# Optimization experiments

Hardware: AMD Instinct MI355X
Metric: run time of the kernel (lower is better)

## Reference

```python
import jax, jax.numpy as jnp
import numpy as np

D = 512          # latent_dim
H = 8            # num_heads
NLAYERS = 8
DFF = 8          # fast_transformers d_ff slot receives num_heads in the repo (kept faithful)
NC = 10          # NUM_CLUSTERS
KMEANS_ITERS = 10
NJ, NF, T, BS = 25, 6, 1024, 16
NCLS, MAXA = 12, 6


def _pe(S, d):
    pos = jnp.arange(S, dtype=jnp.float32)[:, None]
    div = jnp.exp(jnp.arange(0, d, 2, dtype=jnp.float32) * (-np.log(10000.0) / d))
    pe = jnp.zeros((S, d), jnp.float32)
    pe = pe.at[:, 0::2].set(jnp.sin(pos * div))
    pe = pe.at[:, 1::2].set(jnp.cos(pos * div))
    return pe


def _ln(x, g, b, eps=1e-5):
    m = jnp.mean(x, -1, keepdims=True)
    v = jnp.var(x, -1, keepdims=True)
    return (x - m) * jax.lax.rsqrt(v + eps) * g + b


def _clustered_attn_one(q, k, v):
    # q, k, v: (L, Dh). Cluster queries (Lloyd k-means, deterministic init from
    # first NC queries), attend with centroids, broadcast back to queries.
    cent = q[:NC]
    for _ in range(KMEANS_ITERS):
        d = jnp.sum(cent * cent, -1)[None, :] - 2.0 * (q @ cent.T)  # (L, C)
        a = jnp.argmin(d, -1)
        oh = jax.nn.one_hot(a, NC, dtype=q.dtype)                   # (L, C)
        cent = (oh.T @ q) / jnp.maximum(oh.sum(0), 1.0)[:, None]
    d = jnp.sum(cent * cent, -1)[None, :] - 2.0 * (q @ cent.T)
    a = jnp.argmin(d, -1)                                           # (L,)
    temp = 1.0 / np.sqrt(q.shape[-1])
    A = jax.nn.softmax((cent @ k.T) * temp, -1)                     # (C, L)
    return (A @ v)[a]                                               # (L, Dh)


def _layer(z, Wq, bq, Wk, bk, Wv, bv, Wo, bo, g1, c1, g2, c2, W1, b1, W2, b2):
    B, S, d = z.shape
    Dh = d // H
    q = (z @ Wq + bq).reshape(B, S, H, Dh).transpose(0, 2, 1, 3).reshape(B * H, S, Dh)
    k = (z @ Wk + bk).reshape(B, S, H, Dh).transpose(0, 2, 1, 3).reshape(B * H, S, Dh)
    v = (z @ Wv + bv).reshape(B, S, H, Dh).transpose(0, 2, 1, 3).reshape(B * H, S, Dh)
    o = jax.vmap(_clustered_attn_one)(q, k, v)
    o = o.reshape(B, H, S, Dh).transpose(0, 2, 1, 3).reshape(B, S, d)
    z = z + (o @ Wo + bo)                     # post-norm TransformerEncoderLayer
    z = _ln(z, g1, c1)
    y = jax.nn.relu(z @ W1 + b1) @ W2 + b2    # d_ff == num_heads (repo bug, kept)
    return _ln(z + y, g2, c2)


def _forward(x, muQuery, sigmaQuery, mu_w, mu_b, sig_w, sig_b, skel_w, skel_b,
             Wq, bq, Wk, bk, Wv, bv, Wo, bo, g1, c1, g2, c2, W1, b1, W2, b2, y):
    bs, nj, nf, nframes = x.shape
    h = x.transpose(3, 0, 1, 2).reshape(nframes, bs, nj * nf) @ skel_w + skel_b  # (T,B,D)
    mu_enc = muQuery[y].reshape(bs, -1) @ mu_w + mu_b          # (B, D)
    sig_enc = sigmaQuery[y].reshape(bs, -1) @ sig_w + sig_b    # (B, D)
    xseq = jnp.concatenate([mu_enc[None], sig_enc[None], h], 0)  # (S, B, D)
    S = xseq.shape[0]
    xseq = xseq + _pe(S, xseq.shape[-1])[:, None, :]
    z = xseq.transpose(1, 0, 2)  # (B, S, D): attend over the sequence axis
    for i in range(NLAYERS):
        z = _layer(z, Wq[i], bq[i], Wk[i], bk[i], Wv[i], bv[i], Wo[i], bo[i],
                   g1[i], c1[i], g2[i], c2[i], W1[i], b1[i], W2[i], b2[i])
    out = z.transpose(1, 0, 2)  # (S, B, D)
    return out[0], out[1]       # mu, logvar: (B, D) each


def setup_inputs() -> dict:
    key = jax.random.key(0)
    ks = jax.random.split(key, 20)
    s = 0.02
    return {
        "x": jax.random.normal(ks[0], (BS, NJ, NF, T), jnp.float32),
        "y": jax.random.randint(ks[1], (BS, MAXA), 0, NCLS),
        "mask": jnp.ones((BS, T), bool),
        "muQuery": jax.random.normal(ks[2], (NCLS, D), jnp.float32),
        "sigmaQuery": jax.random.normal(ks[3], (NCLS + 1, D), jnp.float32),
        "mu_w": jax.random.normal(ks[4], (D * MAXA, D), jnp.float32) * s,
        "mu_b": jnp.zeros((D,), jnp.float32),
        "sig_w": jax.random.normal(ks[5], (D * MAXA, D), jnp.float32) * s,
        "sig_b": jnp.zeros((D,), jnp.float32),
        "skel_w": jax.random.normal(ks[6], (NJ * NF, D), jnp.float32) * s,
        "skel_b": jnp.zeros((D,), jnp.float32),
        "Wq": jax.random.normal(ks[7], (NLAYERS, D, D), jnp.float32) * s,
        "bq": jnp.zeros((NLAYERS, D), jnp.float32),
        "Wk": jax.random.normal(ks[8], (NLAYERS, D, D), jnp.float32) * s,
        "bk": jnp.zeros((NLAYERS, D), jnp.float32),
        "Wv": jax.random.normal(ks[9], (NLAYERS, D, D), jnp.float32) * s,
        "bv": jnp.zeros((NLAYERS, D), jnp.float32),
        "Wo": jax.random.normal(ks[10], (NLAYERS, D, D), jnp.float32) * s,
        "bo": jnp.zeros((NLAYERS, D), jnp.float32),
        "g1": jnp.ones((NLAYERS, D), jnp.float32),
        "c1": jnp.zeros((NLAYERS, D), jnp.float32),
        "g2": jnp.ones((NLAYERS, D), jnp.float32),
        "c2": jnp.zeros((NLAYERS, D), jnp.float32),
        "W1": jax.random.normal(ks[11], (NLAYERS, D, DFF), jnp.float32) * s,
        "b1": jnp.zeros((NLAYERS, DFF), jnp.float32),
        "W2": jax.random.normal(ks[12], (NLAYERS, DFF, D), jnp.float32) * s,
        "b2": jnp.zeros((NLAYERS, D), jnp.float32),
    }


def reference(x, y, mask, muQuery, sigmaQuery, mu_w, mu_b, sig_w, sig_b,
              skel_w, skel_b, Wq, bq, Wk, bk, Wv, bv, Wo, bo,
              g1, c1, g2, c2, W1, b1, W2, b2):
    del mask  # computed but never passed to the encoder in the original code
    mu, logvar = _forward(x, muQuery, sigmaQuery, mu_w, mu_b, sig_w, sig_b,
                          skel_w, skel_b, Wq, bq, Wk, bk, Wv, bv, Wo, bo,
                          g1, c1, g2, c2, W1, b1, W2, b2, y)
    return mu, logvar
```

## Files before the change

### kernel.cpp

```cpp
#include <hip/hip_runtime.h>
#include <hip/hip_fp16.h>
#include <math.h>

#define D 512
#define H 8
#define DH 64
#define NLAYERS 8
#define DFF 8
#define NC 10
#define KITERS 10
#define SEQ 1026
#define SEQP 1032
#define BATCH 16
#define MR (BATCH*SEQ)
#define NBUF ((size_t)MR * D)
#define DD ((size_t)D * D)
#define NBH (BATCH*H)
#define KSPLIT 64
#define KCH 48

typedef _Float16 f16;
typedef f16 f16x8 __attribute__((ext_vector_type(8)));
typedef float f32x4 __attribute__((ext_vector_type(4)));

__device__ __forceinline__ void split2(float x, float y, unsigned& uh, unsigned& ul) {
    __half hx = __float2half_rn(x), hy = __float2half_rn(y);
    __half lx = __float2half_rn(x - __half2float(hx));
    __half ly = __float2half_rn(y - __half2float(hy));
    uh = (unsigned)__half_as_ushort(hx) | ((unsigned)__half_as_ushort(hy) << 16);
    ul = (unsigned)__half_as_ushort(lx) | ((unsigned)__half_as_ushort(ly) << 16);
}

__device__ __forceinline__ float pe_val(int s, int d) {
    float e = (float)(d & ~1);
    float dv = expf(e * (-9.210340371976184f / 512.0f));
    float ph = (float)s * dv;
    return (d & 1) ? cosf(ph) : sinf(ph);
}

__launch_bounds__(256)
__global__ void convert_w(const float* __restrict__ Wq, const float* __restrict__ Wk,
                          const float* __restrict__ Wv,
                          ushort* __restrict__ whiT, ushort* __restrict__ wloT)
{
    __shared__ float tile[64][65];
    const int tid = threadIdx.x;
    const int k0 = blockIdx.x * 64, n0 = blockIdx.y * 64, m = blockIdx.z;
    const int which = m % 3, lyr = m / 3;
    const float* base;
    switch (which) { case 0: base = Wq; break; case 1: base = Wk; break;
                     default: base = Wv; }
    const float* W = base + (size_t)lyr * DD;
    {
        int r = tid >> 4, c = (tid & 15) * 4;
        #pragma unroll
        for (int p = 0; p < 4; ++p) {
            float4 v = *(const float4*)&W[(size_t)(k0 + r + p*16)*D + n0 + c];
            tile[r + p*16][c]   = v.x; tile[r + p*16][c+1] = v.y;
            tile[r + p*16][c+2] = v.z; tile[r + p*16][c+3] = v.w;
        }
    }
    __syncthreads();
    ushort* ohp = whiT + (size_t)m * DD;
    ushort* olp = wloT + (size_t)m * DD;
    {
        int nl = tid >> 3, kc = (tid & 7) * 8;
        #pragma unroll
        for (int p = 0; p < 2; ++p) {
            int n = nl + p*32;
            uint4 UH, UL;
            split2(tile[kc+0][n], tile[kc+1][n], UH.x, UL.x);
            split2(tile[kc+2][n], tile[kc+3][n], UH.y, UL.y);
            split2(tile[kc+4][n], tile[kc+5][n], UH.z, UL.z);
            split2(tile[kc+6][n], tile[kc+7][n], UH.w, UL.w);
            size_t off = (size_t)(n0 + n)*D + k0 + kc;
            *(uint4*)&ohp[off] = UH;
            *(uint4*)&olp[off] = UL;
        }
    }
}

__launch_bounds__(256)
__global__ void embed_ms_part(const int* __restrict__ y,
    const float* __restrict__ muQ, const float* __restrict__ sigQ,
    const float* __restrict__ mu_w, const float* __restrict__ sig_w,
    float* __restrict__ pbuf)
{
    __shared__ float xs[BATCH][KCH];
    const int tid = threadIdx.x;
    const int kc = blockIdx.x, p = blockIdx.y;
    const float* Q = p ? sigQ : muQ;
    const float* W = p ? sig_w : mu_w;
    for (int i = tid; i < BATCH*KCH; i += 256) {
        int b = i / KCH, k = i - b*KCH;
        int gk = kc*KCH + k;
        int a = y[b*6 + (gk >> 9)];
        xs[b][k] = Q[a*D + (gk & 511)];
    }
    __syncthreads();
    const int n0 = tid*2;
    float a0[BATCH], a1[BATCH];
    #pragma unroll
    for (int b = 0; b < BATCH; ++b) { a0[b] = 0.f; a1[b] = 0.f; }
    #pragma unroll 4
    for (int k = 0; k < KCH; ++k) {
        const float2 wv = *(const float2*)&W[(size_t)(kc*KCH + k)*D + n0];
        #pragma unroll
        for (int b = 0; b < BATCH; ++b) {
            float xv = xs[b][k];
            a0[b] += xv * wv.x;
            a1[b] += xv * wv.y;
        }
    }
    float* pp = pbuf + ((size_t)(p*KSPLIT + kc)*BATCH)*D;
    #pragma unroll
    for (int b = 0; b < BATCH; ++b)
        *(float2*)&pp[(size_t)b*D + n0] = make_float2(a0[b], a1[b]);
}

__launch_bounds__(256)
__global__ void embed_ms_reduce(const float* __restrict__ pbuf,
    const float* __restrict__ mu_b, const float* __restrict__ sig_b,
    float* __restrict__ z)
{
    const int tid = threadIdx.x;
    const int p = blockIdx.x, b = blockIdx.y;
    const float* bb = p ? sig_b : mu_b;
    #pragma unroll
    for (int half = 0; half < 2; ++half) {
        const int d = tid + half*256;
        float s = bb[d];
        const float* pp = pbuf + ((size_t)(p*KSPLIT)*BATCH + b)*D + d;
        #pragma unroll 8
        for (int kc = 0; kc < KSPLIT; ++kc)
            s += pp[(size_t)kc*BATCH*D];
        z[((size_t)b*SEQ + p)*D + d] = s + pe_val(p, d);
    }
}

__launch_bounds__(256)
__global__ void embed_kernel(const float* __restrict__ x,
    const float* __restrict__ skel_w, const float* __restrict__ skel_b,
    float* __restrict__ z)
{
    __shared__ float xin[600];
    const int bx = blockIdx.x, b = blockIdx.y, tid = threadIdx.x;
    const int f0 = bx * 4;
    for (int idx = tid; idx < 600; idx += 256) {
        int i = idx >> 2, ff = idx & 3;
        xin[idx] = x[((size_t)(b*150 + i))*1024 + f0 + ff];
    }
    __syncthreads();
    const float4* x4 = (const float4*)xin;
    for (int dd = 0; dd < 2; ++dd) {
        const int d = tid + dd*256;
        float a0, a1, a2, a3;
        a0 = a1 = a2 = a3 = skel_b[d];
        for (int i = 0; i < 150; ++i) {
            float4 xv = x4[i];
            float w = skel_w[(size_t)i*D + d];
            a0 += xv.x*w; a1 += xv.y*w; a2 += xv.z*w; a3 += xv.w*w;
        }
        float a[4] = {a0, a1, a2, a3};
        #pragma unroll
        for (int ff = 0; ff < 4; ++ff) {
            int s = f0 + ff + 2;
            z[((size_t)b*SEQ + s)*D + d] = a[ff] + pe_val(s, d);
        }
    }
}

__launch_bounds__(256)
__global__ void gemm_qkv(const float* __restrict__ A,
                         const ushort* __restrict__ Bhi_b, const ushort* __restrict__ Blo_b,
                         const float* __restrict__ bq, const float* __restrict__ bk,
                         const float* __restrict__ bv,
                         float* __restrict__ outbase, int M)
{
    __shared__ ushort Ah[128*40], Al[128*40], Bh[128*40], Bl[128*40];
    const int tid = threadIdx.x;
    const int m0 = blockIdx.y * 128, n0 = blockIdx.x * 128;
    const int zz = blockIdx.z;
    const ushort* Bhi = Bhi_b + (size_t)zz * DD;
    const ushort* Blo = Blo_b + (size_t)zz * DD;
    const float* bias = (zz == 0) ? bq : (zz == 1) ? bk : bv;
    float* out = outbase + (size_t)zz * NBUF;
    const int l = tid & 63, wv = tid >> 6;
    const int wr = wv >> 1, wc = wv & 1;

    f32x4 acc[4][4];
    #pragma unroll
    for (int mi = 0; mi < 4; ++mi)
        #pragma unroll
        for (int ni = 0; ni < 4; ++ni) acc[mi][ni] = (f32x4){0.f, 0.f, 0.f, 0.f};

    const int ar_s = tid >> 1, ac_s = (tid & 1) * 16;
    const bool va = (m0 + ar_s) < M;
    const int r0 = (tid*2) >> 2,   kc0 = ((tid*2) & 3) * 8;
    const int r1 = (tid*2+1) >> 2, kc1 = ((tid*2+1) & 3) * 8;
    const float4 fz = make_float4(0.f, 0.f, 0.f, 0.f);

    for (int kt = 0; kt < 16; ++kt) {
        const int kb = kt * 32;
        float4 a0 = fz, a1 = fz, a2 = fz, a3 = fz;
        if (va) {
            const float4* ap = (const float4*)&A[(size_t)(m0 + ar_s)*D + kb + ac_s];
            a0 = ap[0]; a1 = ap[1]; a2 = ap[2]; a3 = ap[3];
        }
        uint4 bh0 = *(const uint4*)&Bhi[(size_t)(n0+r0)*D + kb + kc0];
        uint4 bh1 = *(const uint4*)&Bhi[(size_t)(n0+r1)*D + kb + kc1];
        uint4 bl0 = *(const uint4*)&Blo[(size_t)(n0+r0)*D + kb + kc0];
        uint4 bl1 = *(const uint4*)&Blo[(size_t)(n0+r1)*D + kb + kc1];

        uint4 AH0, AL0, AH1, AL1;
        split2(a0.x, a0.y, AH0.x, AL0.x); split2(a0.z, a0.w, AH0.y, AL0.y);
        split2(a1.x, a1.y, AH0.z, AL0.z); split2(a1.z, a1.w, AH0.w, AL0.w);
        split2(a2.x, a2.y, AH1.x, AL1.x); split2(a2.z, a2.w, AH1.y, AL1.y);
        split2(a3.x, a3.y, AH1.z, AL1.z); split2(a3.z, a3.w, AH1.w, AL1.w);

        if (kt) __syncthreads();
        *(uint4*)&Ah[ar_s*40 + ac_s]     = AH0;
        *(uint4*)&Ah[ar_s*40 + ac_s + 8] = AH1;
        *(uint4*)&Al[ar_s*40 + ac_s]     = AL0;
        *(uint4*)&Al[ar_s*40 + ac_s + 8] = AL1;
        *(uint4*)&Bh[r0*40 + kc0] = bh0;  *(uint4*)&Bh[r1*40 + kc1] = bh1;
        *(uint4*)&Bl[r0*40 + kc0] = bl0;  *(uint4*)&Bl[r1*40 + kc1] = bl1;
        __syncthreads();

        const int ko = (l >> 4) * 8;
        f16x8 bhf[4], blf[4];
        #pragma unroll
        for (int ni = 0; ni < 4; ++ni) {
            int br = wc*64 + ni*16 + (l & 15);
            bhf[ni] = *(const f16x8*)&Bh[br*40 + ko];
            blf[ni] = *(const f16x8*)&Bl[br*40 + ko];
        }
        #pragma unroll
        for (int mi = 0; mi < 4; ++mi) {
            int ar = wr*64 + mi*16 + (l & 15);
            f16x8 ahf = *(const f16x8*)&Ah[ar*40 + ko];
            f16x8 alf = *(const f16x8*)&Al[ar*40 + ko];
            #pragma unroll
            for (int ni = 0; ni < 4; ++ni) {
                acc[mi][ni] = __builtin_amdgcn_mfma_f32_16x16x32_f16(ahf, bhf[ni], acc[mi][ni], 0, 0, 0);
                acc[mi][ni] = __builtin_amdgcn_mfma_f32_16x16x32_f16(ahf, blf[ni], acc[mi][ni], 0, 0, 0);
                acc[mi][ni] = __builtin_amdgcn_mfma_f32_16x16x32_f16(alf, bhf[ni], acc[mi][ni], 0, 0, 0);
            }
        }
    }

    const int col_base = n0 + wc*64 + (l & 15);
    const int row_base = m0 + wr*64 + ((l >> 4) << 2);
    #pragma unroll
    for (int ni = 0; ni < 4; ++ni) {
        const int col = col_base + ni*16;
        const float bv2 = bias[col];
        #pragma unroll
        for (int mi = 0; mi < 4; ++mi) {
            #pragma unroll
            for (int e = 0; e < 4; ++e) {
                const int row = row_base + mi*16 + e;
                if (row >= M) continue;
                float val = acc[mi][ni][e] + bv2;
                int bb = row / SEQ;
                int ss = row - bb*SEQ;
                int hh = col >> 6, dh = col & 63;
                out[((size_t)(bb*H + hh)*SEQ + ss)*DH + dh] = val;
            }
        }
    }
}

__launch_bounds__(1024, 4)
__global__ void attn_kernel(const float* __restrict__ q, const float* __restrict__ kk,
                            const float* __restrict__ v,
                            float* __restrict__ centout, unsigned char* __restrict__ assignout)
{
    __shared__ float At[NC][SEQP];
    __shared__ float cent[NC][DH];
    __shared__ float tailrow[2][DH];
    __shared__ float cnorm[NC];
    __shared__ int   cnt[NC];
    __shared__ int   chg;
    __shared__ unsigned char assign[1028];
    __shared__ float redA[16][NC];
    __shared__ float redB[16][NC];
    __shared__ float Mc[NC];
    __shared__ float Sinv[NC];

    const int tid = threadIdx.x;
    const int wv = tid >> 6, lane = tid & 63;
    const int bh = blockIdx.x;
    const float* qh = q  + (size_t)bh * SEQ * DH;
    const float* kh = kk + (size_t)bh * SEQ * DH;
    const float* vh = v  + (size_t)bh * SEQ * DH;
    float* part = &At[0][0];

    if (tid < NC*DH) ((float*)cent)[tid] = qh[tid];
    if (tid >= NC*DH && tid < NC*DH + 2*DH) ((float*)tailrow)[tid - NC*DH] = qh[1024*DH + (tid - NC*DH)];
    __syncthreads();

    const float4* qrow4 = (const float4*)(qh + (size_t)tid * DH);
    int prev_a = -1, prev_t = -1;

    for (int iter = 0; iter <= KITERS; ++iter) {
        if (tid < NC) {
            float sn = 0.f;
            #pragma unroll
            for (int i = 0; i < 16; ++i) {
                float4 cv = *(const float4*)&cent[tid][i*4];
                sn += cv.x*cv.x + cv.y*cv.y + cv.z*cv.z + cv.w*cv.w;
            }
            cnorm[tid] = sn;
            cnt[tid] = 0;
        }
        if (tid == 0) chg = 0;
        __syncthreads();

        int a_reg;
        {
            float acc[NC];
            #pragma unroll
            for (int c = 0; c < NC; ++c) acc[c] = 0.f;
            #pragma unroll 8
            for (int kq = 0; kq < 16; ++kq) {
                float4 qv = qrow4[kq];
                #pragma unroll
                for (int c = 0; c < NC; ++c) {
                    float4 cv = *(const float4*)&cent[c][kq*4];
                    acc[c] += qv.x*cv.x + qv.y*cv.y + qv.z*cv.z + qv.w*cv.w;
                }
            }
            int best = 0; float bd = 1e30f;
            #pragma unroll
            for (int c = 0; c < NC; ++c) {
                float dd = cnorm[c] - 2.f*acc[c];
                if (dd < bd) { bd = dd; best = c; }
            }
            a_reg = best;
            assign[tid] = (unsigned char)best;
        }
        {
            unsigned long long mm = __ballot(a_reg != prev_a);
            if (lane == 0 && mm) atomicAdd(&chg, 1);
            prev_a = a_reg;
        }
        if (iter < KITERS) {
            #pragma unroll
            for (int c = 0; c < NC; ++c) {
                unsigned long long m = __ballot(a_reg == c);
                if (lane == 0 && m) atomicAdd(&cnt[c], __popcll(m));
            }
        }
        if (tid < 2) {
            int best = 0; float bd = 1e30f;
            #pragma unroll
            for (int c = 0; c < NC; ++c) {
                float acc = 0.f;
                #pragma unroll
                for (int i = 0; i < 64; ++i) acc += tailrow[tid][i]*cent[c][i];
                float dd = cnorm[c] - 2.f*acc;
                if (dd < bd) { bd = dd; best = c; }
            }
            assign[1024 + tid] = (unsigned char)best;
            if (best != prev_t) atomicAdd(&chg, 1);
            prev_t = best;
            if (iter < KITERS) atomicAdd(&cnt[best], 1);
        }
        __syncthreads();
        if (iter == KITERS) break;
        if (chg == 0) break;

        {
            float accq[NC];
            #pragma unroll
            for (int c = 0; c < NC; ++c) accq[c] = 0.f;
            const int s0 = wv * 64;
            #pragma unroll 8
            for (int i = 0; i < 64; ++i) {
                int s = s0 + i;
                float qv = qh[(size_t)s*DH + lane];
                int c = assign[s];
                #pragma unroll
                for (int cc = 0; cc < NC; ++cc) accq[cc] += (cc == c) ? qv : 0.f;
            }
            if (wv < 2) {
                int c = assign[1024 + wv];
                float qv = tailrow[wv][lane];
                #pragma unroll
                for (int cc = 0; cc < NC; ++cc) accq[cc] += (cc == c) ? qv : 0.f;
            }
            #pragma unroll
            for (int c = 0; c < NC; ++c) part[(wv*NC + c)*DH + lane] = accq[c];
        }
        __syncthreads();
        if (tid < NC*DH) {
            int c = tid >> 6;
            float s = 0.f;
            #pragma unroll
            for (int w = 0; w < 16; ++w) s += part[w*(NC*DH) + tid];
            ((float*)cent)[tid] = s / fmaxf((float)cnt[c], 1.f);
        }
        __syncthreads();
    }

    if (tid < 2*DH) ((float*)tailrow)[tid] = kh[1024*DH + tid];
    __syncthreads();

    float lg[NC], lgt[NC];
    {
        const float4* krow4 = (const float4*)(kh + (size_t)tid * DH);
        #pragma unroll
        for (int c = 0; c < NC; ++c) lg[c] = 0.f;
        #pragma unroll 8
        for (int kq = 0; kq < 16; ++kq) {
            float4 kv = krow4[kq];
            #pragma unroll
            for (int c = 0; c < NC; ++c) {
                float4 cv = *(const float4*)&cent[c][kq*4];
                lg[c] += kv.x*cv.x + kv.y*cv.y + kv.z*cv.z + kv.w*cv.w;
            }
        }
        #pragma unroll
        for (int c = 0; c < NC; ++c) lg[c] *= 0.125f;
    }
    if (tid < 2) {
        #pragma unroll
        for (int c = 0; c < NC; ++c) {
            float acc = 0.f;
            #pragma unroll
            for (int i = 0; i < 64; ++i) acc += tailrow[tid][i]*cent[c][i];
            lgt[c] = 0.125f * acc;
        }
    }

    #pragma unroll
    for (int c = 0; c < NC; ++c) {
        float m = lg[c];
        if (tid < 2) m = fmaxf(m, lgt[c]);
        #pragma unroll
        for (int off = 32; off; off >>= 1) m = fmaxf(m, __shfl_xor(m, off, 64));
        if (lane == 0) redA[wv][c] = m;
    }
    __syncthreads();
    if (tid < NC) {
        float m = redA[0][tid];
        #pragma unroll
        for (int w = 1; w < 16; ++w) m = fmaxf(m, redA[w][tid]);
        Mc[tid] = m;
    }
    __syncthreads();
    #pragma unroll
    for (int c = 0; c < NC; ++c) lg[c] = expf(lg[c] - Mc[c]);
    if (tid < 2) {
        #pragma unroll
        for (int c = 0; c < NC; ++c) lgt[c] = expf(lgt[c] - Mc[c]);
    }
    #pragma unroll
    for (int c = 0; c < NC; ++c) {
        float s = lg[c] + ((tid < 2) ? lgt[c] : 0.f);
        #pragma unroll
        for (int off = 32; off; off >>= 1) s += __shfl_xor(s, off, 64);
        if (lane == 0) redB[wv][c] = s;
    }
    __syncthreads();
    if (tid < NC) {
        float s = 0.f;
        #pragma unroll
        for (int w = 0; w < 16; ++w) s += redB[w][tid];
        Sinv[tid] = 1.f / s;
    }
    __syncthreads();
    #pragma unroll
    for (int c = 0; c < NC; ++c) At[c][tid] = lg[c] * Sinv[c];
    if (tid < 2) {
        #pragma unroll
        for (int c = 0; c < NC; ++c) At[c][1024 + tid] = lgt[c] * Sinv[c];
    }
    __syncthreads();

    {
        float accv[NC];
        #pragma unroll
        for (int c = 0; c < NC; ++c) accv[c] = 0.f;
        const int s0 = wv * 64;
        for (int i = 0; i < 64; i += 4) {
            float vv0 = vh[(size_t)(s0+i  )*DH + lane];
            float vv1 = vh[(size_t)(s0+i+1)*DH + lane];
            float vv2 = vh[(size_t)(s0+i+2)*DH + lane];
            float vv3 = vh[(size_t)(s0+i+3)*DH + lane];
            #pragma unroll
            for (int c = 0; c < NC; ++c) {
                float4 av = *(const float4*)&At[c][s0+i];
                accv[c] += av.x*vv0 + av.y*vv1 + av.z*vv2 + av.w*vv3;
            }
        }
        if (wv < 2) {
            int s = 1024 + wv;
            float vv = vh[(size_t)s*DH + lane];
            #pragma unroll
            for (int c = 0; c < NC; ++c) accv[c] += At[c][s] * vv;
        }
        __syncthreads();
        #pragma unroll
        for (int c = 0; c < NC; ++c) part[(wv*NC + c)*DH + lane] = accv[c];
    }
    __syncthreads();
    if (tid < NC*DH) {
        float s = 0.f;
        #pragma unroll
        for (int w = 0; w < 16; ++w) s += part[w*(NC*DH) + tid];
        centout[(size_t)bh*(NC*DH) + tid] = s;
    }
    for (int i = tid; i < SEQ; i += 1024)
        assignout[(size_t)bh*SEQP + i] = assign[i];
}

__launch_bounds__(256)
__global__ void pproj_kernel(const float* __restrict__ centout, const float* __restrict__ Wo,
                             float* __restrict__ P)
{
    __shared__ float cs[NC][DH];
    const int tid = threadIdx.x;
    const int bh = blockIdx.x, h = bh & 7;
    const int n = blockIdx.y * 256 + tid;
    for (int i = tid; i < NC*DH; i += 256) ((float*)cs)[i] = centout[(size_t)bh*(NC*DH) + i];
    __syncthreads();
    float acc[NC];
    #pragma unroll
    for (int c = 0; c < NC; ++c) acc[c] = 0.f;
    #pragma unroll 8
    for (int d = 0; d < DH; ++d) {
        float wv = Wo[(size_t)(h*DH + d)*D + n];
        #pragma unroll
        for (int c = 0; c < NC; ++c) acc[c] += cs[c][d] * wv;
    }
    #pragma unroll
    for (int c = 0; c < NC; ++c)
        P[((size_t)bh*NC + c)*D + n] = acc[c];
}

__launch_bounds__(256)
__global__ void ffn_ln_kernel(float* __restrict__ z,
    const float* __restrict__ P, const unsigned char* __restrict__ assignbuf,
    const float* __restrict__ bo,
    const float* __restrict__ g1, const float* __restrict__ c1,
    const float* __restrict__ W1, const float* __restrict__ b1,
    const float* __restrict__ W2, const float* __restrict__ b2,
    const float* __restrict__ g2, const float* __restrict__ c2)
{
    __shared__ float red[8];
    __shared__ float redh[4][DFF];
    const int row = blockIdx.x, tid = threadIdx.x;
    const int lane = tid & 63, wid = tid >> 6;
    const int b = row / SEQ, s = row - b*SEQ;

    float x0 = z[(size_t)row*D + tid]       + bo[tid];
    float x1 = z[(size_t)row*D + tid + 256] + bo[tid + 256];
    #pragma unroll
    for (int h = 0; h < H; ++h) {
        int a = assignbuf[(size_t)(b*H + h)*SEQP + s];
        const float* Pr = P + ((size_t)(b*H + h)*NC + a)*D;
        x0 += Pr[tid];
        x1 += Pr[tid + 256];
    }

    float sm = x0 + x1, ss = x0*x0 + x1*x1;
    #pragma unroll
    for (int off = 32; off; off >>= 1) {
        sm += __shfl_xor(sm, off, 64);
        ss += __shfl_xor(ss, off, 64);
    }
    if (lane == 0) { red[wid] = sm; red[4 + wid] = ss; }
    __syncthreads();
    float tot  = red[0] + red[1] + red[2] + red[3];
    float tot2 = red[4] + red[5] + red[6] + red[7];
    float mean = tot * (1.f/512.f);
    float var  = tot2 * (1.f/512.f) - mean*mean;
    float rstd = rsqrtf(var + 1e-5f);
    float za = (x0 - mean)*rstd*g1[tid]       + c1[tid];
    float zb = (x1 - mean)*rstd*g1[tid + 256] + c1[tid + 256];

    float p[DFF];
    #pragma unroll
    for (int j = 0; j < DFF; ++j)
        p[j] = za * W1[(size_t)tid*DFF + j] + zb * W1[(size_t)(tid+256)*DFF + j];
    #pragma unroll
    for (int off = 32; off; off >>= 1)
        #pragma unroll
        for (int j = 0; j < DFF; ++j) p[j] += __shfl_xor(p[j], off, 64);
    if (lane == 0) {
        #pragma unroll
        for (int j = 0; j < DFF; ++j) redh[wid][j] = p[j];
    }
    __syncthreads();
    float hv[DFF];
    #pragma unroll
    for (int j = 0; j < DFF; ++j)
        hv[j] = fmaxf(redh[0][j] + redh[1][j] + redh[2][j] + redh[3][j] + b1[j], 0.f);
    float y0 = b2[tid], y1 = b2[tid + 256];
    #pragma unroll
    for (int j = 0; j < DFF; ++j) {
        y0 += hv[j] * W2[(size_t)j*D + tid];
        y1 += hv[j] * W2[(size_t)j*D + tid + 256];
    }
    float t0 = za + y0, t1 = zb + y1;
    float s2 = t0 + t1, ss2 = t0*t0 + t1*t1;
    #pragma unroll
    for (int off = 32; off; off >>= 1) {
        s2  += __shfl_xor(s2,  off, 64);
        ss2 += __shfl_xor(ss2, off, 64);
    }
    if (lane == 0) { red[wid] = s2; red[4 + wid] = ss2; }
    __syncthreads();
    float tt  = red[0] + red[1] + red[2] + red[3];
    float tt2 = red[4] + red[5] + red[6] + red[7];
    float m2 = tt * (1.f/512.f);
    float v2 = tt2 * (1.f/512.f) - m2*m2;
    float rstd2 = rsqrtf(v2 + 1e-5f);
    float* zo = z + (size_t)row * D;
    zo[tid]       = (t0 - m2)*rstd2*g2[tid]       + c2[tid];
    zo[tid + 256] = (t1 - m2)*rstd2*g2[tid + 256] + c2[tid + 256];
}

__launch_bounds__(256)
__global__ void extract_kernel(const float* __restrict__ z, float* __restrict__ out) {
    int i = blockIdx.x * 256 + threadIdx.x;
    if (i >= 2*BATCH*D) return;
    int half = i >> 13;
    int j = i & 8191;
    int b = j >> 9, d = j & 511;
    out[i] = z[((size_t)b*SEQ + half)*D + d];
}

extern "C" void kernel_launch(void* const* d_in, const int* in_sizes, int n_in,
                              void* d_out, int out_size, void* d_ws, size_t ws_size,
                              hipStream_t stream)
{
    const float* x      = (const float*)d_in[0];
    const int*   y      = (const int*)  d_in[1];
    const float* muQ    = (const float*)d_in[3];
    const float* sigQ   = (const float*)d_in[4];
    const float* mu_w   = (const float*)d_in[5];
    const float* mu_b   = (const float*)d_in[6];
    const float* sig_w  = (const float*)d_in[7];
    const float* sig_b  = (const float*)d_in[8];
    const float* skel_w = (const float*)d_in[9];
    const float* skel_b = (const float*)d_in[10];
    const float* Wq     = (const float*)d_in[11];
    const float* bq     = (const float*)d_in[12];
    const float* Wk     = (const float*)d_in[13];
    const float* bk     = (const float*)d_in[14];
    const float* Wv     = (const float*)d_in[15];
    const float* bv     = (const float*)d_in[16];
    const float* Wo     = (const float*)d_in[17];
    const float* bo     = (const float*)d_in[18];
    const float* g1     = (const float*)d_in[19];
    const float* c1     = (const float*)d_in[20];
    const float* g2     = (const float*)d_in[21];
    const float* c2     = (const float*)d_in[22];
    const float* W1     = (const float*)d_in[23];
    const float* b1     = (const float*)d_in[24];
    const float* W2     = (const float*)d_in[25];
    const float* b2     = (const float*)d_in[26];

    float*  z    = (float*)d_ws;
    float*  qb   = z  + NBUF;
    float*  kb   = qb + NBUF;
    float*  vb   = kb + NBUF;
    ushort* wThi = (ushort*)(vb + NBUF);
    ushort* wTlo = wThi + 24*DD;
    float*  centbuf  = (float*)(wTlo + 24*DD);
    float*  P        = centbuf + (size_t)NBH*NC*DH;
    unsigned char* assignbuf = (unsigned char*)(P + (size_t)NBH*NC*D);
    float*  pbuf = (float*)(assignbuf + (size_t)NBH*SEQP);

    convert_w<<<dim3(8, 8, 24), 256, 0, stream>>>(Wq, Wk, Wv, wThi, wTlo);

    embed_ms_part<<<dim3(KSPLIT, 2), 256, 0, stream>>>(y, muQ, sigQ, mu_w, sig_w, pbuf);
    embed_ms_reduce<<<dim3(2, BATCH), 256, 0, stream>>>(pbuf, mu_b, sig_b, z);
    embed_kernel<<<dim3(256, BATCH), 256, 0, stream>>>(x, skel_w, skel_b, z);

    for (int l = 0; l < NLAYERS; ++l) {
        gemm_qkv<<<dim3(4, 129, 3), 256, 0, stream>>>(
            z, wThi + (size_t)l*3*DD, wTlo + (size_t)l*3*DD,
            bq + l*D, bk + l*D, bv + l*D, qb, MR);
        attn_kernel<<<NBH, 1024, 0, stream>>>(qb, kb, vb, centbuf, assignbuf);
        pproj_kernel<<<dim3(NBH, 2), 256, 0, stream>>>(centbuf, Wo + (size_t)l*DD, P);
        ffn_ln_kernel<<<MR, 256, 0, stream>>>(z, P, assignbuf, bo + l*D,
            g1 + (size_t)l*D, c1 + (size_t)l*D,
            W1 + (size_t)l*D*DFF, b1 + (size_t)l*DFF,
            W2 + (size_t)l*DFF*D, b2 + (size_t)l*D,
            g2 + (size_t)l*D, c2 + (size_t)l*D);
    }
    extract_kernel<<<64, 256, 0, stream>>>(z, (float*)d_out);

    (void)in_sizes; (void)n_in; (void)out_size; (void)ws_size;
}
```

Baseline: 4.401 ms.

## Compute k-means query-centroid distances with split-fp16 MFMA and shuffle argmin

```diff
diff --git a/kernel.cpp b/kernel.cpp
--- a/kernel.cpp
+++ b/kernel.cpp
@@ -31,6 +31,20 @@
     ul = (unsigned)__half_as_ushort(lx) | ((unsigned)__half_as_ushort(ly) << 16);
 }
 
+__device__ __forceinline__ void sp1(float a, f16& h, f16& l) {
+    h = (f16)a;
+    l = (f16)(a - (float)h);
+}
+#define SP8(U0, U1, HV, LV) { f16 th, tl; \
+    sp1(U0.x, th, tl); HV[0] = th; LV[0] = tl; \
+    sp1(U0.y, th, tl); HV[1] = th; LV[1] = tl; \
+    sp1(U0.z, th, tl); HV[2] = th; LV[2] = tl; \
+    sp1(U0.w, th, tl); HV[3] = th; LV[3] = tl; \
+    sp1(U1.x, th, tl); HV[4] = th; LV[4] = tl; \
+    sp1(U1.y, th, tl); HV[5] = th; LV[5] = tl; \
+    sp1(U1.z, th, tl); HV[6] = th; LV[6] = tl; \
+    sp1(U1.w, th, tl); HV[7] = th; LV[7] = tl; }
+
 __device__ __forceinline__ float pe_val(int s, int d) {
     float e = (float)(d & ~1);
     float dv = expf(e * (-9.210340371976184f / 512.0f));
@@ -278,11 +292,13 @@
 {
     __shared__ float At[NC][SEQP];
     __shared__ float cent[NC][DH];
+    __shared__ ushort centh[16][72];
+    __shared__ ushort centl[16][72];
     __shared__ float tailrow[2][DH];
-    __shared__ float cnorm[NC];
+    __shared__ float cnorm16[16];
     __shared__ int   cnt[NC];
     __shared__ int   chg;
-    __shared__ unsigned char assign[1028];
+    __shared__ unsigned char assign[1040];
     __shared__ float redA[16][NC];
     __shared__ float redB[16][NC];
     __shared__ float Mc[NC];
@@ -298,74 +314,85 @@
 
     if (tid < NC*DH) ((float*)cent)[tid] = qh[tid];
     if (tid >= NC*DH && tid < NC*DH + 2*DH) ((float*)tailrow)[tid - NC*DH] = qh[1024*DH + (tid - NC*DH)];
-    __syncthreads();
-
-    const float4* qrow4 = (const float4*)(qh + (size_t)tid * DH);
-    int prev_a = -1, prev_t = -1;
+    for (int i = tid; i < 1040; i += 1024) assign[i] = 255;
+    for (int i = tid; i < 16*72; i += 1024) { (&centh[0][0])[i] = 0; (&centl[0][0])[i] = 0; }
+    __syncthreads();
 
     for (int iter = 0; iter <= KITERS; ++iter) {
-        if (tid < NC) {
-            float sn = 0.f;
-            #pragma unroll
-            for (int i = 0; i < 16; ++i) {
-                float4 cv = *(const float4*)&cent[tid][i*4];
-                sn += cv.x*cv.x + cv.y*cv.y + cv.z*cv.z + cv.w*cv.w;
+        if (tid < 16) {
+            float sn = 1e30f;
+            if (tid < NC) {
+                sn = 0.f;
+                #pragma unroll
+                for (int i = 0; i < 16; ++i) {
+                    float4 cv = *(const float4*)&cent[tid][i*4];
+                    sn += cv.x*cv.x + cv.y*cv.y + cv.z*cv.z + cv.w*cv.w;
+                }
+                cnt[tid] = 0;
             }
-            cnorm[tid] = sn;
-            cnt[tid] = 0;
+            cnorm16[tid] = sn;
+        }
+        if (tid < 640) {
+            int c = tid >> 6, d = tid & 63;
+            float vv = cent[c][d];
+            __half hh = __float2half_rn(vv);
+            centh[c][d] = __half_as_ushort(hh);
+            centl[c][d] = __half_as_ushort(__float2half_rn(vv - __half2float(hh)));
         }
         if (tid == 0) chg = 0;
         __syncthreads();
 
-        int a_reg;
         {
-            float acc[NC];
-            #pragma unroll
-            for (int c = 0; c < NC; ++c) acc[c] = 0.f;
-            #pragma unroll 8
-            for (int kq = 0; kq < 16; ++kq) {
-                float4 qv = qrow4[kq];
-                #pragma unroll
-                for (int c = 0; c < NC; ++c) {
-                    float4 cv = *(const float4*)&cent[c][kq*4];
-                    acc[c] += qv.x*cv.x + qv.y*cv.y + qv.z*cv.z + qv.w*cv.w;
+            const int bc = lane & 15, kg = lane >> 4;
+            f16x8 B_h0 = *(const f16x8*)&centh[bc][kg*8];
+            f16x8 B_l0 = *(const f16x8*)&centl[bc][kg*8];
+            f16x8 B_h1 = *(const f16x8*)&centh[bc][32 + kg*8];
+            f16x8 B_l1 = *(const f16x8*)&centl[bc][32 + kg*8];
+            const float cn = cnorm16[bc];
+            const int ntiles = (wv == 15) ? 5 : 4;
+            for (int t = 0; t < ntiles; ++t) {
+                const int s0 = (wv*4 + t) * 16;
+                const int arow = s0 + bc;
+                const float4* ap = (const float4*)(qh + (size_t)arow*DH + kg*8);
+                float4 u0 = ap[0], u1 = ap[1];
+                const float4* ap2 = (const float4*)(qh + (size_t)arow*DH + 32 + kg*8);
+                float4 u2 = ap2[0], u3 = ap2[1];
+                f16x8 A_h0, A_l0, A_h1, A_l1;
+                SP8(u0, u1, A_h0, A_l0)
+                SP8(u2, u3, A_h1, A_l1)
+                f32x4 acc = (f32x4){0.f, 0.f, 0.f, 0.f};
+                acc = __builtin_amdgcn_mfma_f32_16x16x32_f16(A_h0, B_h0, acc, 0, 0, 0);
+                acc = __builtin_amdgcn_mfma_f32_16x16x32_f16(A_l0, B_h0, acc, 0, 0, 0);
+                acc = __builtin_amdgcn_mfma_f32_16x16x32_f16(A_h0, B_l0, acc, 0, 0, 0);
+                acc = __builtin_amdgcn_mfma_f32_16x16x32_f16(A_h1, B_h1, acc, 0, 0, 0);
+                acc = __builtin_amdgcn_mfma_f32_16x16x32_f16(A_l1, B_h1, acc, 0, 0, 0);
+                acc = __builtin_amdgcn_mfma_f32_16x16x32_f16(A_h1, B_l1, acc, 0, 0, 0);
+                int w0, w1, w2, w3;
+#define ARGMIN_E(EIDX, WOUT) { \
+                float dv = cn - 2.f*acc[EIDX]; int cv = bc; \
+                _Pragma("unroll") \
+                for (int off = 1; off < 16; off <<= 1) { \
+                    float d2 = __shfl_xor(dv, off, 64); \
+                    int   c2 = __shfl_xor(cv, off, 64); \
+                    if (d2 < dv || (d2 == dv && c2 < cv)) { dv = d2; cv = c2; } \
+                } \
+                WOUT = cv; }
+                ARGMIN_E(0, w0) ARGMIN_E(1, w1) ARGMIN_E(2, w2) ARGMIN_E(3, w3)
+#undef ARGMIN_E
+                if (bc == 0) {
+                    const int sb = s0 + kg*4;
+                    #pragma unroll
+                    for (int e = 0; e < 4; ++e) {
+                        int s = sb + e;
+                        if (s < SEQ) {
+                            int nw = (e == 0) ? w0 : (e == 1) ? w1 : (e == 2) ? w2 : w3;
+                            if ((int)assign[s] != nw) atomicAdd(&chg, 1);
+                            assign[s] = (unsigned char)nw;
+                            atomicAdd(&cnt[nw], 1);
+                        }
+                    }
                 }
             }
-            int best = 0; float bd = 1e30f;
-            #pragma unroll
-            for (int c = 0; c < NC; ++c) {
-                float dd = cnorm[c] - 2.f*acc[c];
-                if (dd < bd) { bd = dd; best = c; }
-            }
-            a_reg = best;
-            assign[tid] = (unsigned char)best;
-        }
-        {
-            unsigned long long mm = __ballot(a_reg != prev_a);
-            if (lane == 0 && mm) atomicAdd(&chg, 1);
-            prev_a = a_reg;
-        }
-        if (iter < KITERS) {
-            #pragma unroll
-            for (int c = 0; c < NC; ++c) {
-                unsigned long long m = __ballot(a_reg == c);
-                if (lane == 0 && m) atomicAdd(&cnt[c], __popcll(m));
-            }
-        }
-        if (tid < 2) {
-            int best = 0; float bd = 1e30f;
-            #pragma unroll
-            for (int c = 0; c < NC; ++c) {
-                float acc = 0.f;
-                #pragma unroll
-                for (int i = 0; i < 64; ++i) acc += tailrow[tid][i]*cent[c][i];
-                float dd = cnorm[c] - 2.f*acc;
-                if (dd < bd) { bd = dd; best = c; }
-            }
-            assign[1024 + tid] = (unsigned char)best;
-            if (best != prev_t) atomicAdd(&chg, 1);
-            prev_t = best;
-            if (iter < KITERS) atomicAdd(&cnt[best], 1);
         }
         __syncthreads();
         if (iter == KITERS) break;
```

After: 4.790 ms. 1.09x slower.
